# Optimization experiments

Measured on AMD Instinct MI355X. Metric: run time of the kernel, lower is better.

Reference implementation:

```python
import math
import jax, jax.numpy as jnp
import numpy as np

D_MODEL = 256
D2 = 2 * D_MODEL
NHEADS = 8
NLAYERS = 6
FFN = 1024
Q, B, S = 300, 16, 1024


def _ln(x, eps=1e-5):
    m = jnp.mean(x, axis=-1, keepdims=True)
    v = jnp.mean((x - m) ** 2, axis=-1, keepdims=True)
    return (x - m) / jnp.sqrt(v + eps)


def _mlp2(x, W1, b1, W2, b2):
    return jnp.maximum(x @ W1 + b1, 0.0) @ W2 + b2


def _sine_embed(pos, d_model):
    # pos: [Q, B, 2] -> [Q, B, d_model]
    fd = d_model // 2
    dim_t = jnp.arange(fd, dtype=jnp.float32)
    dim_t = 10000.0 ** (2.0 * jnp.floor(dim_t / 2.0) / fd)
    scale = 2.0 * math.pi
    px = (pos[:, :, 0] * scale)[:, :, None] / dim_t
    py = (pos[:, :, 1] * scale)[:, :, None] / dim_t

    def inter(p):
        q, b, _ = p.shape
        return jnp.stack((jnp.sin(p[:, :, 0::2]), jnp.cos(p[:, :, 1::2])), axis=3).reshape(q, b, -1)

    return jnp.concatenate((inter(py), inter(px)), axis=2)


def _pairwise_iou(b):
    # b: [B, Q, 4] xyxy -> [B, Q, Q]
    area = (b[..., 2] - b[..., 0]) * (b[..., 3] - b[..., 1])
    lt = jnp.maximum(b[:, :, None, :2], b[:, None, :, :2])
    rb = jnp.minimum(b[:, :, None, 2:], b[:, None, :, 2:])
    wh = jnp.clip(rb - lt, 0.0)
    inter = wh[..., 0] * wh[..., 1]
    union = area[:, :, None] + area[:, None, :] - inter
    return inter / union


def _mha(q, k, v, Wq, Wk, Wv, Wo, bias=None):
    # q: [L,B,D], k/v: [S,B,D]
    L, Bb, D = q.shape
    Ss = k.shape[0]
    hd = D // NHEADS
    qh = (q @ Wq).reshape(L, Bb, NHEADS, hd).transpose(1, 2, 0, 3)  # [B,H,L,hd]
    kh = (k @ Wk).reshape(Ss, Bb, NHEADS, hd).transpose(1, 2, 0, 3)
    vh = (v @ Wv).reshape(Ss, Bb, NHEADS, hd).transpose(1, 2, 0, 3)
    logits = jnp.einsum('bhqd,bhkd->bhqk', qh, kh) / jnp.sqrt(jnp.float32(hd))
    if bias is not None:
        logits = logits + bias[:, None]  # broadcast over heads
    a = jax.nn.softmax(logits, axis=-1)
    o = jnp.einsum('bhqk,bhkd->bhqd', a, vh).transpose(2, 0, 1, 3).reshape(L, Bb, D)
    return o @ Wo


def setup_inputs() -> dict:
    key = jax.random.key(0)
    ks = iter(jax.random.split(key, 40))
    f32 = jnp.float32
    d = D_MODEL
    sc = 0.02
    inp = {
        'tgt': jax.random.normal(next(ks), (Q, B, D2), f32),
        'memory': jax.random.normal(next(ks), (S, B, D2), f32),
        'pos': jax.random.normal(next(ks), (S, B, D2), f32),
        'query_pos': jax.random.normal(next(ks), (Q, B, d), f32),
        # query_scale MLP (d->d->d)
        'qs_W1': jax.random.normal(next(ks), (d, d), f32) * sc, 'qs_b1': jnp.zeros((d,), f32),
        'qs_W2': jax.random.normal(next(ks), (d, d), f32) * sc, 'qs_b2': jnp.zeros((d,), f32),
        # ref_point_head MLP (d->d->2)
        'rp_W1': jax.random.normal(next(ks), (d, d), f32) * sc, 'rp_b1': jnp.zeros((d,), f32),
        'rp_W2': jax.random.normal(next(ks), (d, 2), f32) * sc, 'rp_b2': jnp.zeros((2,), f32),
        # bbox_embed_func MLP (d->d->4)
        'bb_W1': jax.random.normal(next(ks), (d, d), f32) * sc, 'bb_b1': jnp.zeros((d,), f32),
        'bb_W2': jax.random.normal(next(ks), (d, 4), f32) * sc, 'bb_b2': jnp.zeros((4,), f32),
    }
    for name in ['sa_Wq', 'sa_Wk', 'sa_Wv', 'sa_Wo', 'ca_Wq', 'ca_Wk', 'ca_Wv', 'ca_Wo']:
        inp[name] = jax.random.normal(next(ks), (NLAYERS, D2, D2), f32) * sc
    inp['ff_W1'] = jax.random.normal(next(ks), (NLAYERS, D2, FFN), f32) * sc
    inp['ff_b1'] = jnp.zeros((NLAYERS, FFN), f32)
    inp['ff_W2'] = jax.random.normal(next(ks), (NLAYERS, FFN, D2), f32) * sc
    inp['ff_b2'] = jnp.zeros((NLAYERS, D2), f32)
    return inp


def reference(tgt, memory, pos, query_pos,
              qs_W1, qs_b1, qs_W2, qs_b2,
              rp_W1, rp_b1, rp_W2, rp_b2,
              bb_W1, bb_b1, bb_W2, bb_b2,
              sa_Wq, sa_Wk, sa_Wv, sa_Wo,
              ca_Wq, ca_Wk, ca_Wv, ca_Wo,
              ff_W1, ff_b1, ff_W2, ff_b2):
    d = D_MODEL
    output = tgt
    ref_before = _mlp2(query_pos, rp_W1, rp_b1, rp_W2, rp_b2)          # [Q,B,2]
    reference_points = jax.nn.sigmoid(ref_before).transpose(1, 0, 2)   # [B,Q,2]
    qp2 = jnp.concatenate((query_pos, query_pos), axis=-1)             # [Q,B,2d]
    for l in range(NLAYERS):
        obj_center = reference_points.transpose(1, 0, 2)               # [Q,B,2]
        pos_transform = _mlp2(output[..., d:], qs_W1, qs_b1, qs_W2, qs_b2)
        qs = _sine_embed(obj_center, d) * pos_transform                # [Q,B,d]
        tmp = _mlp2(output[..., d:], bb_W1, bb_b1, bb_W2, bb_b2)       # [Q,B,4]
        tmp = tmp.at[..., :2].add(ref_before)
        coord = jax.nn.sigmoid(tmp)                                    # cxcywh
        cx, cy, w, h = coord[..., 0], coord[..., 1], coord[..., 2], coord[..., 3]
        boxes = jnp.stack((cx - 0.5 * w, cy - 0.5 * h, cx + 0.5 * w, cy + 0.5 * h),
                          axis=-1).transpose(1, 0, 2)                  # [B,Q,4]
        gious = jax.lax.stop_gradient(_pairwise_iou(boxes))            # [B,Q,Q]
        cs = (cx + cy).transpose(1, 0)                                 # [B,Q]
        cxcys = jax.lax.stop_gradient((cs[:, :, None] > cs[:, None, :]).astype(output.dtype))
        bias = gious + cxcys                                            # [B,Q,Q]
        qs2 = jnp.concatenate((qs, qs), axis=-1)                        # [Q,B,2d]
        # self-attention with giou/cxcy bias
        qsa = output + qp2
        sa = _mha(qsa, qsa, output, sa_Wq[l], sa_Wk[l], sa_Wv[l], sa_Wo[l], bias=bias)
        output = _ln(output + sa)
        # cross-attention, sine-modulated query
        ca = _mha(output + qp2 + qs2, memory + pos, memory,
                  ca_Wq[l], ca_Wk[l], ca_Wv[l], ca_Wo[l])
        output = _ln(output + ca)
        ff = jnp.maximum(output @ ff_W1[l] + ff_b1[l], 0.0) @ ff_W2[l] + ff_b2[l]
        output = _ln(output + ff)
    return output[None]  # [1,Q,B,2d]
```

## Files before the change

### kernel.cpp

```cpp
#include <hip/hip_runtime.h>
#include <cmath>

#define QLEN 300
#define BATCH 16
#define SLEN 1024
#define DM 256
#define DD 512
#define FFND 1024
#define NQROWS (QLEN*BATCH)
#define NMROWS (SLEN*BATCH)
#define LQPAD 304
#define SAKPAD 320

typedef __attribute__((ext_vector_type(8))) short short8;
typedef __attribute__((ext_vector_type(4))) float f32x4;
typedef __attribute__((ext_vector_type(4))) unsigned short ushort4_;

__device__ __forceinline__ float sigmoidf_(float x){ return 1.f/(1.f+expf(-x)); }

__device__ __forceinline__ unsigned short f2bf(float x){
  unsigned u = __float_as_uint(x);
  unsigned r = (u + 0x7FFFu + ((u >> 16) & 1u)) >> 16;
  return (unsigned short)r;
}
__device__ __forceinline__ float bf2f(unsigned short u){
  return __uint_as_float(((unsigned)u) << 16);
}

__device__ __forceinline__ void gload16(const void* g, void* l) {
  __builtin_amdgcn_global_load_lds((const __attribute__((address_space(1))) unsigned int*)g,
                                   (__attribute__((address_space(3))) unsigned int*)l, 16, 0, 0);
}

__global__ __launch_bounds__(256) void transpose_cvt(
    const float* __restrict__ W, unsigned short* __restrict__ Wt, int K, int N)
{
  __shared__ float T[32][33];
  int n0 = blockIdx.x*32, k0 = blockIdx.y*32;
  size_t zo = (size_t)blockIdx.z * K * N;
  int tx = threadIdx.x & 31, ty = threadIdx.x >> 5;
  #pragma unroll
  for (int j = 0; j < 32; j += 8)
    T[ty+j][tx] = W[zo + (size_t)(k0+ty+j)*N + n0+tx];
  __syncthreads();
  #pragma unroll
  for (int j = 0; j < 32; j += 8)
    Wt[zo + (size_t)(n0+ty+j)*K + k0+tx] = f2bf(T[tx][ty+j]);
}

template<int BM, int OUTMODE, bool RELU>
__global__ __launch_bounds__(256) void gemm2(
    const unsigned short* __restrict__ Ab, const unsigned short* __restrict__ Wt,
    const float* __restrict__ bias, void* __restrict__ Cptr,
    int M, int N, int K, int lda, int Laux)
{
  __shared__ __align__(16) unsigned short As[2][BM*64];
  __shared__ __align__(16) unsigned short Bs[2][128*64];
  const int tid = threadIdx.x;
  const int w = tid >> 6, lane = tid & 63;
  const int bm = blockIdx.y*BM, bn = blockIdx.x*128;
  const int wm = w >> 1, wn = w & 1;
  const int c = lane & 15, hi = lane >> 4;
  constexpr int MR = BM/32;
  f32x4 acc[MR][4] = {};
  const int lrow8 = lane >> 3;
  const int lcol  = ((lane & 7) ^ lrow8) << 3;
  const int nt = K >> 6;

  auto stage = [&](int buf, int k0) {
    #pragma unroll
    for (int it = 0; it < BM/32; ++it) {
      int r = it*32 + w*8;
      gload16(&Ab[(size_t)(bm + r + lrow8)*lda + k0 + lcol], &As[buf][r*64]);
    }
    #pragma unroll
    for (int it = 0; it < 4; ++it) {
      int r = it*32 + w*8;
      gload16(&Wt[(size_t)(bn + r + lrow8)*K + k0 + lcol], &Bs[buf][r*64]);
    }
  };

  stage(0, 0);
  for (int t = 0; t < nt; ++t) {
    const int cur = t & 1;
    if (t + 1 < nt) {
      stage(cur ^ 1, (t+1) << 6);
      if constexpr (BM == 64) asm volatile("s_waitcnt vmcnt(6)" ::: "memory");
      else                    asm volatile("s_waitcnt vmcnt(8)" ::: "memory");
    } else {
      asm volatile("s_waitcnt vmcnt(0)" ::: "memory");
    }
    __builtin_amdgcn_s_barrier();
    #pragma unroll
    for (int ks = 0; ks < 2; ++ks) {
      short8 a[MR], bf[4];
      #pragma unroll
      for (int mr = 0; mr < MR; ++mr) {
        int m = wm*(BM/2) + mr*16 + c;
        a[mr] = *reinterpret_cast<const short8*>(&As[cur][m*64 + ((ks*32 + hi*8) ^ ((m&7)<<3))]);
      }
      #pragma unroll
      for (int nr = 0; nr < 4; ++nr) {
        int n = wn*64 + nr*16 + c;
        bf[nr] = *reinterpret_cast<const short8*>(&Bs[cur][n*64 + ((ks*32 + hi*8) ^ ((n&7)<<3))]);
      }
      #pragma unroll
      for (int mr = 0; mr < MR; ++mr)
        #pragma unroll
        for (int nr = 0; nr < 4; ++nr)
          acc[mr][nr] = __builtin_amdgcn_mfma_f32_16x16x32_bf16(a[mr], bf[nr], acc[mr][nr], 0, 0, 0);
    }
    asm volatile("s_waitcnt lgkmcnt(0)" ::: "memory");
    __builtin_amdgcn_sched_barrier(0);
    __builtin_amdgcn_s_barrier();
  }
  #pragma unroll
  for (int mr = 0; mr < MR; ++mr) {
    #pragma unroll
    for (int nr = 0; nr < 4; ++nr) {
      int colg = bn + wn*64 + nr*16 + c;
      float bv = bias ? bias[colg] : 0.f;
      #pragma unroll
      for (int r = 0; r < 4; ++r) {
        int rowg = bm + wm*(BM/2) + mr*16 + hi*4 + r;
        float v = acc[mr][nr][r] + bv;
        if (RELU) v = fmaxf(v, 0.f);
        if (OUTMODE == 0) {
          ((float*)Cptr)[(size_t)rowg*N + colg] = v;
        } else if (OUTMODE == 1) {
          ((unsigned short*)Cptr)[(size_t)rowg*N + colg] = f2bf(v);
        } else {
          int bb = rowg & 15, row = rowg >> 4, h = colg >> 6, dl = colg & 63;
          ((unsigned short*)Cptr)[(((size_t)bb*8 + h)*Laux + row)*64 + dl] = f2bf(v);
        }
      }
    }
  }
}

template<int BM>
__global__ __launch_bounds__(256) void gemm2_vt(
    const unsigned short* __restrict__ Ab, const unsigned short* __restrict__ Wt,
    unsigned short* __restrict__ VT, int Lsrc, int K, int lda, int Lkpad, int tilesPerB)
{
  __shared__ __align__(16) unsigned short As[2][BM*64];
  __shared__ __align__(16) unsigned short Bs[2][128*64];
  const int tid = threadIdx.x;
  const int w = tid >> 6, lane = tid & 63;
  const int b = blockIdx.y / tilesPerB;
  const int qt = (blockIdx.y - b*tilesPerB) * BM;
  const int bn = blockIdx.x*128;
  const int wm = w >> 1, wn = w & 1;
  const int c = lane & 15, hi = lane >> 4;
  constexpr int MR = BM/32;
  f32x4 acc[MR][4] = {};
  const int lrow8 = lane >> 3;
  const int lcol  = ((lane & 7) ^ lrow8) << 3;
  const int nt = K >> 6;

  auto stage = [&](int buf, int k0) {
    #pragma unroll
    for (int it = 0; it < BM/32; ++it) {
      int r = it*32 + w*8;
      int q = qt + r + lrow8; if (q > Lsrc-1) q = Lsrc-1;
      gload16(&Ab[(size_t)(q*BATCH + b)*lda + k0 + lcol], &As[buf][r*64]);
    }
    #pragma unroll
    for (int it = 0; it < 4; ++it) {
      int r = it*32 + w*8;
      gload16(&Wt[(size_t)(bn + r + lrow8)*K + k0 + lcol], &Bs[buf][r*64]);
    }
  };

  stage(0, 0);
  for (int t = 0; t < nt; ++t) {
    const int cur = t & 1;
    if (t + 1 < nt) {
      stage(cur ^ 1, (t+1) << 6);
      if constexpr (BM == 64) asm volatile("s_waitcnt vmcnt(6)" ::: "memory");
      else                    asm volatile("s_waitcnt vmcnt(8)" ::: "memory");
    } else {
      asm volatile("s_waitcnt vmcnt(0)" ::: "memory");
    }
    __builtin_amdgcn_s_barrier();
    #pragma unroll
    for (int ks = 0; ks < 2; ++ks) {
      short8 a[MR], bf[4];
      #pragma unroll
      for (int mr = 0; mr < MR; ++mr) {
        int m = wm*(BM/2) + mr*16 + c;
        a[mr] = *reinterpret_cast<const short8*>(&As[cur][m*64 + ((ks*32 + hi*8) ^ ((m&7)<<3))]);
      }
      #pragma unroll
      for (int nr = 0; nr < 4; ++nr) {
        int n = wn*64 + nr*16 + c;
        bf[nr] = *reinterpret_cast<const short8*>(&Bs[cur][n*64 + ((ks*32 + hi*8) ^ ((n&7)<<3))]);
      }
      #pragma unroll
      for (int mr = 0; mr < MR; ++mr)
        #pragma unroll
        for (int nr = 0; nr < 4; ++nr)
          acc[mr][nr] = __builtin_amdgcn_mfma_f32_16x16x32_bf16(a[mr], bf[nr], acc[mr][nr], 0, 0, 0);
    }
    asm volatile("s_waitcnt lgkmcnt(0)" ::: "memory");
    __builtin_amdgcn_sched_barrier(0);
    __builtin_amdgcn_s_barrier();
  }
  #pragma unroll
  for (int mr = 0; mr < MR; ++mr) {
    #pragma unroll
    for (int nr = 0; nr < 4; ++nr) {
      int colg = bn + wn*64 + nr*16 + c;
      int h = colg >> 6, dl = colg & 63;
      int q0 = qt + wm*(BM/2) + mr*16 + hi*4;
      ushort4_ pack;
      #pragma unroll
      for (int r = 0; r < 4; ++r) pack[r] = f2bf(acc[mr][nr][r]);
      *reinterpret_cast<ushort4_*>(&VT[((size_t)(b*8 + h)*64 + dl)*Lkpad + q0]) = pack;
    }
  }
}

template<int AMODE, bool OUTBF16, bool RELU>
__global__ __launch_bounds__(256) void gemm_mfma(
    const void* __restrict__ Aptr, const float* __restrict__ A2,
    const unsigned short* __restrict__ Wt, const float* __restrict__ bias,
    void* __restrict__ Cptr, int M, int N, int K, int lda)
{
  __shared__ __align__(16) unsigned short As[64][72];
  __shared__ __align__(16) unsigned short Bs[64][72];
  const int tid = threadIdx.x;
  const int bm = blockIdx.y*64, bn = blockIdx.x*64;
  const int w = tid >> 6, lane = tid & 63;
  const int wm = w >> 1, wn = w & 1;
  const int c = lane & 15, hi = lane >> 4;
  const int sr = tid >> 3, sk = (tid & 7) * 8;
  f32x4 acc[2][2] = {};
  for (int k0 = 0; k0 < K; k0 += 64) {
    #pragma unroll
    for (int it = 0; it < 2; ++it) {
      int m = sr + it*32;
      if (AMODE == 0) {
        const unsigned short* Ab = (const unsigned short*)Aptr;
        short8 v = *reinterpret_cast<const short8*>(&Ab[(size_t)(bm+m)*lda + k0 + sk]);
        *reinterpret_cast<short8*>(&As[m][sk]) = v;
      } else {
        const float* Af = (const float*)Aptr;
        size_t base = (size_t)(bm+m)*lda + k0 + sk;
        float4 f0 = *reinterpret_cast<const float4*>(&Af[base]);
        float4 f1 = *reinterpret_cast<const float4*>(&Af[base+4]);
        short8 v;
        v[0]=(short)f2bf(f0.x); v[1]=(short)f2bf(f0.y); v[2]=(short)f2bf(f0.z); v[3]=(short)f2bf(f0.w);
        v[4]=(short)f2bf(f1.x); v[5]=(short)f2bf(f1.y); v[6]=(short)f2bf(f1.z); v[7]=(short)f2bf(f1.w);
        *reinterpret_cast<short8*>(&As[m][sk]) = v;
      }
      short8 bv = *reinterpret_cast<const short8*>(&Wt[(size_t)(bn+m)*K + k0 + sk]);
      *reinterpret_cast<short8*>(&Bs[m][sk]) = bv;
    }
    __syncthreads();
    #pragma unroll
    for (int ks = 0; ks < 2; ++ks) {
      short8 a0 = *reinterpret_cast<const short8*>(&As[wm*32 + c][ks*32 + hi*8]);
      short8 a1 = *reinterpret_cast<const short8*>(&As[wm*32 + 16 + c][ks*32 + hi*8]);
      short8 b0 = *reinterpret_cast<const short8*>(&Bs[wn*32 + c][ks*32 + hi*8]);
      short8 b1 = *reinterpret_cast<const short8*>(&Bs[wn*32 + 16 + c][ks*32 + hi*8]);
      acc[0][0] = __builtin_amdgcn_mfma_f32_16x16x32_bf16(a0, b0, acc[0][0], 0, 0, 0);
      acc[0][1] = __builtin_amdgcn_mfma_f32_16x16x32_bf16(a0, b1, acc[0][1], 0, 0, 0);
      acc[1][0] = __builtin_amdgcn_mfma_f32_16x16x32_bf16(a1, b0, acc[1][0], 0, 0, 0);
      acc[1][1] = __builtin_amdgcn_mfma_f32_16x16x32_bf16(a1, b1, acc[1][1], 0, 0, 0);
    }
    __syncthreads();
  }
  #pragma unroll
  for (int mf = 0; mf < 2; ++mf) {
    #pragma unroll
    for (int nf = 0; nf < 2; ++nf) {
      int colg = bn + wn*32 + nf*16 + c;
      float bv = bias ? bias[colg] : 0.f;
      #pragma unroll
      for (int r = 0; r < 4; ++r) {
        int rowg = bm + wm*32 + mf*16 + hi*4 + r;
        float v = acc[mf][nf][r] + bv;
        if (RELU) v = fmaxf(v, 0.f);
        if (OUTBF16) ((unsigned short*)Cptr)[(size_t)rowg*N + colg] = f2bf(v);
        else         ((float*)Cptr)[(size_t)rowg*N + colg] = v;
      }
    }
  }
}

template<bool HAS_BIAS, bool MASK, int NS>
__global__ __launch_bounds__(256) void attn2(
    const unsigned short* __restrict__ Qh, const unsigned short* __restrict__ Kh,
    const unsigned short* __restrict__ VT, const float* __restrict__ bias,
    unsigned short* __restrict__ Ob, unsigned short* __restrict__ Opart, float* __restrict__ MLpart,
    int Lq, int Lk, int Lkpad)
{
  __shared__ __align__(16) unsigned short Ks[2][64*64];
  __shared__ __align__(16) unsigned short Vs[2][64*64];
  __shared__ __align__(16) unsigned short Pl[4][16][72];
  const int tid = threadIdx.x;
  const int w = tid >> 6, lane = tid & 63;
  const int c = lane & 15, hi = lane >> 4;
  const int bh = blockIdx.x;
  const int qt = blockIdx.y * 64;
  const int sp = blockIdx.z;
  const int b = bh >> 3;
  const int lrow8 = lane >> 3;
  const int lcol  = ((lane & 7) ^ lrow8) << 3;

  const int nt_tot = (Lk + 63) >> 6;
  const int t0 = (nt_tot * sp) / NS;
  const int t1 = (nt_tot * (sp + 1)) / NS;

  int qrow = qt + w*16 + c; if (qrow > Lq-1) qrow = Lq-1;
  const unsigned short* qptr = Qh + ((size_t)bh*Lq + qrow)*64;
  short8 qf0 = *reinterpret_cast<const short8*>(qptr + hi*8);
  short8 qf1 = *reinterpret_cast<const short8*>(qptr + 32 + hi*8);

  float m_ = -1e30f, l_ = 0.f;
  f32x4 accO[4] = {};
  const int qbase = qt + w*16 + hi*4;

  auto stageKV = [&](int buf, int kt) {
    #pragma unroll
    for (int it = 0; it < 2; ++it) {
      int r = it*32 + w*8;
      int kr = kt + r + lrow8; if (MASK && kr > Lk-1) kr = Lk-1;
      gload16(&Kh[((size_t)bh*Lk + kr)*64 + lcol], &Ks[buf][r*64]);
    }
    #pragma unroll
    for (int it = 0; it < 2; ++it) {
      int r = it*32 + w*8;
      gload16(&VT[((size_t)bh*64 + r + lrow8)*Lkpad + kt + lcol], &Vs[buf][r*64]);
    }
  };

  stageKV(0, t0 << 6);
  for (int t = t0; t < t1; ++t) {
    const int cur = (t - t0) & 1;
    const int kt = t << 6;
    float4 bs4[4];
    if (HAS_BIAS) {
      #pragma unroll
      for (int g = 0; g < 4; ++g)
        bs4[g] = *reinterpret_cast<const float4*>(
            &bias[((size_t)b*Lq + qrow)*Lk + kt + g*16 + hi*4]);
    }
    if (t + 1 < t1) {
      stageKV(cur ^ 1, (t+1) << 6);
      asm volatile("s_waitcnt vmcnt(4)" ::: "memory");
    } else {
      asm volatile("s_waitcnt vmcnt(0)" ::: "memory");
    }
    __builtin_amdgcn_s_barrier();
    f32x4 s[4] = {};
    #pragma unroll
    for (int g = 0; g < 4; ++g) {
      int m = g*16 + c;
      short8 kb0 = *reinterpret_cast<const short8*>(&Ks[cur][m*64 + ((hi*8)      ^ ((m&7)<<3))]);
      short8 kb1 = *reinterpret_cast<const short8*>(&Ks[cur][m*64 + ((32 + hi*8) ^ ((m&7)<<3))]);
      s[g] = __builtin_amdgcn_mfma_f32_16x16x32_bf16(kb0, qf0, s[g], 0, 0, 0);
      s[g] = __builtin_amdgcn_mfma_f32_16x16x32_bf16(kb1, qf1, s[g], 0, 0, 0);
    }
    float tmax = -1e30f;
    #pragma unroll
    for (int g = 0; g < 4; ++g) {
      #pragma unroll
      for (int r = 0; r < 4; ++r) {
        float v = s[g][r] * 0.125f;
        if (HAS_BIAS) v += ((const float*)&bs4[g])[r];
        if (MASK && (kt + g*16 + hi*4 + r >= Lk)) v = -1e30f;
        s[g][r] = v;
        tmax = fmaxf(tmax, v);
      }
    }
    tmax = fmaxf(tmax, __shfl_xor(tmax, 16));
    tmax = fmaxf(tmax, __shfl_xor(tmax, 32));
    float newm = fmaxf(m_, tmax);
    float corr = __expf(m_ - newm);
    m_ = newm;
    float psum = 0.f;
    #pragma unroll
    for (int g = 0; g < 4; ++g) {
      ushort4_ pp;
      #pragma unroll
      for (int r = 0; r < 4; ++r) {
        float e = __expf(s[g][r] - newm);
        psum += e;
        pp[r] = f2bf(e);
      }
      *reinterpret_cast<ushort4_*>(&Pl[w][c][g*16 + hi*4]) = pp;
    }
    psum += __shfl_xor(psum, 16);
    psum += __shfl_xor(psum, 32);
    l_ = l_*corr + psum;
    float corr4[4];
    #pragma unroll
    for (int r = 0; r < 4; ++r) corr4[r] = __shfl(corr, hi*4 + r);
    #pragma unroll
    for (int dg = 0; dg < 4; ++dg)
      #pragma unroll
      for (int r = 0; r < 4; ++r) accO[dg][r] *= corr4[r];
    #pragma unroll
    for (int ks = 0; ks < 2; ++ks) {
      short8 pa = *reinterpret_cast<const short8*>(&Pl[w][c][ks*32 + hi*8]);
      #pragma unroll
      for (int dg = 0; dg < 4; ++dg) {
        int n = dg*16 + c;
        short8 vb = *reinterpret_cast<const short8*>(&Vs[cur][n*64 + ((ks*32 + hi*8) ^ ((n&7)<<3))]);
        accO[dg] = __builtin_amdgcn_mfma_f32_16x16x32_bf16(pa, vb, accO[dg], 0, 0, 0);
      }
    }
    asm volatile("s_waitcnt lgkmcnt(0)" ::: "memory");
    __builtin_amdgcn_sched_barrier(0);
    __builtin_amdgcn_s_barrier();
  }
  if (NS == 1) {
    float l4[4];
    #pragma unroll
    for (int r = 0; r < 4; ++r) l4[r] = __shfl(l_, hi*4 + r);
    #pragma unroll
    for (int r = 0; r < 4; ++r) {
      int qg = qbase + r;
      if (qg < Lq) {
        float inv = 1.f / l4[r];
        int h = bh & 7;
        #pragma unroll
        for (int dg = 0; dg < 4; ++dg)
          Ob[((size_t)qg*BATCH + b)*DD + h*64 + 16*dg + c] = f2bf(accO[dg][r] * inv);
      }
    }
  } else {
    int qc = qt + w*16 + c;
    if (hi == 0 && qc < Lq) {
      size_t rowml = ((size_t)sp*128 + bh)*LQPAD + qc;
      MLpart[rowml*2]     = m_;
      MLpart[rowml*2 + 1] = l_;
    }
    #pragma unroll
    for (int r = 0; r < 4; ++r) {
      int qg = qbase + r;
      if (qg < Lq) {
        size_t rowo = ((size_t)sp*128 + bh)*LQPAD + qg;
        #pragma unroll
        for (int dg = 0; dg < 4; ++dg)
          Opart[rowo*64 + dg*16 + c] = f2bf(accO[dg][r]);
      }
    }
  }
}

__global__ __launch_bounds__(256) void attn_reduce(
    const unsigned short* __restrict__ Opart, const float* __restrict__ MLpart,
    unsigned short* __restrict__ Ob, int Lq)
{
  int w = threadIdx.x >> 6, lane = threadIdx.x & 63;
  int pair = blockIdx.x*4 + w;
  if (pair >= 128*Lq) return;
  int bh = pair / Lq, q = pair - bh*Lq;
  size_t r0 = (size_t)bh*LQPAD + q;
  size_t r1 = (size_t)(128 + bh)*LQPAD + q;
  float m0 = MLpart[r0*2], l0 = MLpart[r0*2+1];
  float m1 = MLpart[r1*2], l1 = MLpart[r1*2+1];
  float M = fmaxf(m0, m1);
  float w0 = __expf(m0 - M), w1 = __expf(m1 - M);
  float o = w0*bf2f(Opart[r0*64 + lane]) + w1*bf2f(Opart[r1*64 + lane]);
  float l = w0*l0 + w1*l1;
  int b = bh >> 3, h = bh & 7;
  Ob[((size_t)q*BATCH + b)*DD + h*64 + lane] = f2bf(o / l);
}

__global__ __launch_bounds__(256) void gemm_f32(
    const float* __restrict__ A, const float* __restrict__ A2,
    const float* __restrict__ W, const float* __restrict__ bias,
    float* __restrict__ C, int M, int N, int K, int lda, int relu)
{
  __shared__ __align__(16) float As[16][68];
  __shared__ __align__(16) float Bs[16][68];
  const int tid = threadIdx.x;
  const int bm = blockIdx.y * 64, bn = blockIdx.x * 64;
  const int tx = tid & 15, ty = tid >> 4;
  const int ar = tid >> 4, ac = tid & 15;
  const int bk = tid >> 6, bnn = tid & 63;
  float acc[4][4] = {};
  for (int k0 = 0; k0 < K; k0 += 16) {
    #pragma unroll
    for (int i = 0; i < 4; ++i) {
      int row = ar + i*16;
      float v = A[(size_t)(bm+row)*lda + (k0+ac)];
      if (A2) v += A2[(size_t)(bm+row)*lda + (k0+ac)];
      As[ac][row] = v;
    }
    #pragma unroll
    for (int i = 0; i < 4; ++i) {
      int kk = bk + i*4;
      Bs[kk][bnn] = W[(size_t)(k0+kk)*N + (bn+bnn)];
    }
    __syncthreads();
    #pragma unroll
    for (int k = 0; k < 16; ++k) {
      float4 a4 = *reinterpret_cast<const float4*>(&As[k][ty*4]);
      float4 b4 = *reinterpret_cast<const float4*>(&Bs[k][tx*4]);
      float a[4] = {a4.x,a4.y,a4.z,a4.w};
      float bb[4] = {b4.x,b4.y,b4.z,b4.w};
      #pragma unroll
      for (int i=0;i<4;++i)
        #pragma unroll
        for (int j=0;j<4;++j)
          acc[i][j] = fmaf(a[i], bb[j], acc[i][j]);
// ... 115 lines not shown
  float4 p0 = *reinterpret_cast<const float4*>(pos+base);
  float4 p1 = *reinterpret_cast<const float4*>(pos+base+4);
  short8 s1, s2;
  s1[0]=(short)f2bf(a0.x+p0.x); s1[1]=(short)f2bf(a0.y+p0.y); s1[2]=(short)f2bf(a0.z+p0.z); s1[3]=(short)f2bf(a0.w+p0.w);
  s1[4]=(short)f2bf(a1.x+p1.x); s1[5]=(short)f2bf(a1.y+p1.y); s1[6]=(short)f2bf(a1.z+p1.z); s1[7]=(short)f2bf(a1.w+p1.w);
  s2[0]=(short)f2bf(a0.x); s2[1]=(short)f2bf(a0.y); s2[2]=(short)f2bf(a0.z); s2[3]=(short)f2bf(a0.w);
  s2[4]=(short)f2bf(a1.x); s2[5]=(short)f2bf(a1.y); s2[6]=(short)f2bf(a1.z); s2[7]=(short)f2bf(a1.w);
  *reinterpret_cast<short8*>(mb+base)  = s1;
  *reinterpret_cast<short8*>(mvb+base) = s2;
}

__global__ __launch_bounds__(256) void ln_residual(float* __restrict__ X, const float* __restrict__ Y,
                                                   unsigned short* __restrict__ Xb)
{
  int row = blockIdx.x, tid = threadIdx.x;
  size_t base = (size_t)row*DD;
  float v0 = X[base+tid]     + Y[base+tid];
  float v1 = X[base+tid+256] + Y[base+tid+256];
  float s = v0+v1, sq = v0*v0+v1*v1;
  for (int off = 32; off; off >>= 1) { s += __shfl_down(s,off); sq += __shfl_down(sq,off); }
  __shared__ float ss[4], ssq[4];
  int wid = tid>>6, lane = tid&63;
  if (lane==0){ ss[wid]=s; ssq[wid]=sq; }
  __syncthreads();
  if (tid==0){
    float a=ss[0]+ss[1]+ss[2]+ss[3], bsum=ssq[0]+ssq[1]+ssq[2]+ssq[3];
    float mean = a*(1.f/DD);
    float var  = bsum*(1.f/DD) - mean*mean;
    ss[0]=mean; ssq[0]=rsqrtf(fmaxf(var,0.f)+1e-5f);
  }
  __syncthreads();
  float mean = ss[0], inv = ssq[0];
  float o0 = (v0-mean)*inv, o1 = (v1-mean)*inv;
  X[base+tid]     = o0;  Xb[base+tid]     = f2bf(o0);
  X[base+tid+256] = o1;  Xb[base+tid+256] = f2bf(o1);
}

__global__ void init_x(const float* __restrict__ t, float* __restrict__ X,
                       unsigned short* __restrict__ Xb, int n)
{
  int idx = blockIdx.x*blockDim.x + threadIdx.x;
  if (idx < n){ float v = t[idx]; X[idx]=v; Xb[idx]=f2bf(v); }
}

__global__ void copy_f32(const float* __restrict__ src, float* __restrict__ dst, int n)
{
  int idx = blockIdx.x*blockDim.x + threadIdx.x;
  if (idx < n) dst[idx] = src[idx];
}

extern "C" void kernel_launch(void* const* d_in, const int* in_sizes, int n_in,
                              void* d_out, int out_size, void* d_ws, size_t ws_size,
                              hipStream_t stream)
{
  const float* tgt       = (const float*)d_in[0];
  const float* memory    = (const float*)d_in[1];
  const float* pos       = (const float*)d_in[2];
  const float* query_pos = (const float*)d_in[3];
  const float* qs_W1 = (const float*)d_in[4];  const float* qs_b1 = (const float*)d_in[5];
  const float* qs_W2 = (const float*)d_in[6];  const float* qs_b2 = (const float*)d_in[7];
  const float* rp_W1 = (const float*)d_in[8];  const float* rp_b1 = (const float*)d_in[9];
  const float* rp_W2 = (const float*)d_in[10]; const float* rp_b2 = (const float*)d_in[11];
  const float* bb_W1 = (const float*)d_in[12]; const float* bb_b1 = (const float*)d_in[13];
  const float* bb_W2 = (const float*)d_in[14]; const float* bb_b2 = (const float*)d_in[15];
  const float* sa_Wq = (const float*)d_in[16]; const float* sa_Wk = (const float*)d_in[17];
  const float* sa_Wv = (const float*)d_in[18]; const float* sa_Wo = (const float*)d_in[19];
  const float* ca_Wq = (const float*)d_in[20]; const float* ca_Wk = (const float*)d_in[21];
  const float* ca_Wv = (const float*)d_in[22]; const float* ca_Wo = (const float*)d_in[23];
  const float* ff_W1 = (const float*)d_in[24]; const float* ff_b1 = (const float*)d_in[25];
  const float* ff_W2 = (const float*)d_in[26]; const float* ff_b2 = (const float*)d_in[27];

  float* F = (float*)d_ws;
  size_t o = 0;
  float* X    = F + o; o += (size_t)NQROWS*DD;
  float* RES  = F + o; o += (size_t)NQROWS*DD;
  float* SINE = F + o; o += (size_t)NQROWS*DM;
  float* PT   = F + o; o += (size_t)NQROWS*DM;
  float* BIAS = F + o; o += (size_t)BATCH*QLEN*QLEN;
  float* REFB = F + o; o += (size_t)NQROWS*2;
  float* T4   = F + o; o += (size_t)NQROWS*4;
  float* BOX  = F + o; o += (size_t)NQROWS*4;
  float* CS   = F + o; o += (size_t)NQROWS;
  float* ML   = F + o; o += (size_t)2*128*LQPAD*2;
  float* T256 = RES;
  unsigned short* U = (unsigned short*)(F + o);
  size_t u = 0;
  unsigned short* Xb   = U + u; u += (size_t)NQROWS*DD;
  unsigned short* QIN  = U + u; u += (size_t)NQROWS*DD;
  unsigned short* PQb  = U + u; u += (size_t)NQROWS*DD;
  unsigned short* PKb  = U + u; u += (size_t)NMROWS*DD;
  unsigned short* PVb  = U + u; u += (size_t)NMROWS*DD;
  unsigned short* VTsa = U + u; u += (size_t)128*64*SAKPAD;
  unsigned short* OPARTU = U + u; u += (size_t)2*128*LQPAD*64;
  unsigned short* T256b= U + u; u += (size_t)NQROWS*DM;
  unsigned short* MEMb = U + u; u += (size_t)NMROWS*DD;
  unsigned short* MEMVb= U + u; u += (size_t)NMROWS*DD;
  unsigned short* WtSq = U + u; u += (size_t)6*DD*DD;
  unsigned short* WtSk = U + u; u += (size_t)6*DD*DD;
  unsigned short* WtSv = U + u; u += (size_t)6*DD*DD;
  unsigned short* WtSo = U + u; u += (size_t)6*DD*DD;
  unsigned short* WtCq = U + u; u += (size_t)6*DD*DD;
  unsigned short* WtCk = U + u; u += (size_t)6*DD*DD;
  unsigned short* WtCv = U + u; u += (size_t)6*DD*DD;
  unsigned short* WtCo = U + u; u += (size_t)6*DD*DD;
  unsigned short* WtF1 = U + u; u += (size_t)6*DD*FFND;
  unsigned short* WtF2 = U + u; u += (size_t)6*DD*FFND;
  unsigned short* WtQ1 = U + u; u += (size_t)DM*DM;
  unsigned short* WtQ2 = U + u; u += (size_t)DM*DM;
  unsigned short* WtB1 = U + u; u += (size_t)DM*DM;
  unsigned short* AOb  = QIN;
  unsigned short* HIDb = PKb;
  if (ws_size < o*sizeof(float) + u*sizeof(unsigned short)) return;

  dim3 B256(256);
  const int nTotal = NQROWS*DD;

  transpose_cvt<<<dim3(16,16,6), B256, 0, stream>>>(sa_Wq, WtSq, DD, DD);
  transpose_cvt<<<dim3(16,16,6), B256, 0, stream>>>(sa_Wk, WtSk, DD, DD);
  transpose_cvt<<<dim3(16,16,6), B256, 0, stream>>>(sa_Wv, WtSv, DD, DD);
  transpose_cvt<<<dim3(16,16,6), B256, 0, stream>>>(sa_Wo, WtSo, DD, DD);
  transpose_cvt<<<dim3(16,16,6), B256, 0, stream>>>(ca_Wq, WtCq, DD, DD);
  transpose_cvt<<<dim3(16,16,6), B256, 0, stream>>>(ca_Wk, WtCk, DD, DD);
  transpose_cvt<<<dim3(16,16,6), B256, 0, stream>>>(ca_Wv, WtCv, DD, DD);
  transpose_cvt<<<dim3(16,16,6), B256, 0, stream>>>(ca_Wo, WtCo, DD, DD);
  transpose_cvt<<<dim3(32,16,6), B256, 0, stream>>>(ff_W1, WtF1, DD, FFND);
  transpose_cvt<<<dim3(16,32,6), B256, 0, stream>>>(ff_W2, WtF2, FFND, DD);
  transpose_cvt<<<dim3(8,8,1),  B256, 0, stream>>>(qs_W1, WtQ1, DM, DM);
  transpose_cvt<<<dim3(8,8,1),  B256, 0, stream>>>(qs_W2, WtQ2, DM, DM);
  transpose_cvt<<<dim3(8,8,1),  B256, 0, stream>>>(bb_W1, WtB1, DM, DM);

  init_x<<<dim3((nTotal+255)/256), B256, 0, stream>>>(tgt, X, Xb, nTotal);
  cvt_mem<<<dim3(NMROWS*DD/8/256), B256, 0, stream>>>(memory, pos, MEMb, MEMVb);
  gemm_f32<<<dim3(DM/64, NQROWS/64), B256, 0, stream>>>(query_pos, nullptr, rp_W1, rp_b1, T256, NQROWS, DM, DM, DM, 1);
  gemm_skinny<<<dim3(NQROWS/4), B256, 0, stream>>>(T256, rp_W2, rp_b2, REFB, NQROWS, 2, DM, DM);
  sine_embed_kernel<<<dim3((NQROWS*DM+255)/256), B256, 0, stream>>>(REFB, SINE);

  const int nredu = (128*QLEN + 3) / 4;
  const int qtiles = (QLEN + 63) / 64;
  for (int l = 0; l < 6; ++l) {
    const size_t wo = (size_t)l*DD*DD, fo = (size_t)l*DD*FFND;
    const float* fb1 = ff_b1 + (size_t)l*FFND;
    const float* fb2 = ff_b2 + (size_t)l*DD;

    gemm_mfma<0,true,true ><<<dim3(DM/64, NQROWS/64), B256, 0, stream>>>(Xb+DM, nullptr, WtQ1, qs_b1, T256b, NQROWS, DM, DM, DD);
    gemm_mfma<0,false,false><<<dim3(DM/64, NQROWS/64), B256, 0, stream>>>(T256b, nullptr, WtQ2, qs_b2, PT, NQROWS, DM, DM, DM);
    gemm_mfma<0,false,true ><<<dim3(DM/64, NQROWS/64), B256, 0, stream>>>(Xb+DM, nullptr, WtB1, bb_b1, T256, NQROWS, DM, DM, DD);
    gemm_skinny<<<dim3(NQROWS/4), B256, 0, stream>>>(T256, bb_W2, bb_b2, T4, NQROWS, 4, DM, DM);
    boxes_kernel<<<dim3((NQROWS+255)/256), B256, 0, stream>>>(T4, REFB, BOX, CS);
    bias_kernel<<<dim3((BATCH*QLEN*QLEN+255)/256), B256, 0, stream>>>(BOX, CS, BIAS);

    add_qp2<<<dim3((nTotal+255)/256), B256, 0, stream>>>(X, query_pos, QIN);
    gemm2<64,2,false><<<dim3(DD/128, NQROWS/64), B256, 0, stream>>>(QIN, WtSq+wo, nullptr, PQb, NQROWS, DD, DD, DD, QLEN);
    gemm2<64,2,false><<<dim3(DD/128, NQROWS/64), B256, 0, stream>>>(QIN, WtSk+wo, nullptr, PKb, NQROWS, DD, DD, DD, QLEN);
    gemm2_vt<64><<<dim3(DD/128, BATCH*5), B256, 0, stream>>>(Xb, WtSv+wo, VTsa, QLEN, DD, DD, SAKPAD, 5);
    attn2<true,true,2><<<dim3(128, qtiles, 2), B256, 0, stream>>>(PQb, PKb, VTsa, BIAS, nullptr, OPARTU, ML, QLEN, QLEN, SAKPAD);
    attn_reduce<<<dim3(nredu), B256, 0, stream>>>(OPARTU, ML, AOb, QLEN);
    gemm2<64,0,false><<<dim3(DD/128, NQROWS/64), B256, 0, stream>>>(AOb, WtSo+wo, nullptr, RES, NQROWS, DD, DD, DD, 0);
    ln_residual<<<dim3(NQROWS), B256, 0, stream>>>(X, RES, Xb);

    caq_kernel<<<dim3((nTotal+255)/256), B256, 0, stream>>>(X, query_pos, SINE, PT, QIN);
    gemm2<64,2,false><<<dim3(DD/128, NQROWS/64), B256, 0, stream>>>(QIN, WtCq+wo, nullptr, PQb, NQROWS, DD, DD, DD, QLEN);
    gemm2<128,2,false><<<dim3(DD/128, NMROWS/128), B256, 0, stream>>>(MEMb,  WtCk+wo, nullptr, PKb, NMROWS, DD, DD, DD, SLEN);
    gemm2_vt<128><<<dim3(DD/128, BATCH*8), B256, 0, stream>>>(MEMVb, WtCv+wo, PVb, SLEN, DD, DD, SLEN, 8);
    attn2<false,false,2><<<dim3(128, qtiles, 2), B256, 0, stream>>>(PQb, PKb, PVb, nullptr, nullptr, OPARTU, ML, QLEN, SLEN, SLEN);
    attn_reduce<<<dim3(nredu), B256, 0, stream>>>(OPARTU, ML, AOb, QLEN);
    gemm2<64,0,false><<<dim3(DD/128, NQROWS/64), B256, 0, stream>>>(AOb, WtCo+wo, nullptr, RES, NQROWS, DD, DD, DD, 0);
    ln_residual<<<dim3(NQROWS), B256, 0, stream>>>(X, RES, Xb);

    gemm2<64,1,true ><<<dim3(FFND/128, NQROWS/64), B256, 0, stream>>>(Xb, WtF1+fo, fb1, HIDb, NQROWS, FFND, DD, DD, 0);
    gemm2<64,0,false><<<dim3(DD/128, NQROWS/64), B256, 0, stream>>>(HIDb, WtF2+fo, fb2, RES, NQROWS, DD, FFND, FFND, 0);
    ln_residual<<<dim3(NQROWS), B256, 0, stream>>>(X, RES, Xb);
  }

  copy_f32<<<dim3((nTotal+255)/256), B256, 0, stream>>>(X, (float*)d_out, out_size);
}
```

Measured before the change: 1.767 ms.

## Fuse Q/K projections and query MLP first layers, shrink GEMM tiles, add MFMA priority

Self-attention Q and K projection weights are packed into one interleaved matrix so a single GEMM writes both head-major outputs, and attention takes per-batch stride and offset parameters to read them. The qs/bb first-layer MLPs are merged into one split-output GEMM with a concatenated bias. Several N=512 GEMMs switch to a 32-row tile to launch more blocks, and attention raises wave priority around its MFMA sections. This removes kernel launches and re-reads of the input in exchange for new indexing paths; the BM=32 path's staging and waitcnt correctness is unverified.

```diff
diff --git a/kernel.cpp b/kernel.cpp
--- a/kernel.cpp
+++ b/kernel.cpp
@@ -33,19 +33,29 @@
 }
 
 __global__ __launch_bounds__(256) void transpose_cvt(
-    const float* __restrict__ W, unsigned short* __restrict__ Wt, int K, int N)
+    const float* __restrict__ W, unsigned short* __restrict__ Wt, int K, int N,
+    size_t zsrc, size_t zdst)
 {
   __shared__ float T[32][33];
   int n0 = blockIdx.x*32, k0 = blockIdx.y*32;
-  size_t zo = (size_t)blockIdx.z * K * N;
+  size_t zs = (size_t)blockIdx.z * zsrc;
+  size_t zd = (size_t)blockIdx.z * zdst;
   int tx = threadIdx.x & 31, ty = threadIdx.x >> 5;
   #pragma unroll
   for (int j = 0; j < 32; j += 8)
-    T[ty+j][tx] = W[zo + (size_t)(k0+ty+j)*N + n0+tx];
+    T[ty+j][tx] = W[zs + (size_t)(k0+ty+j)*N + n0+tx];
   __syncthreads();
   #pragma unroll
   for (int j = 0; j < 32; j += 8)
-    Wt[zo + (size_t)(n0+ty+j)*K + k0+tx] = f2bf(T[tx][ty+j]);
+    Wt[zd + (size_t)(n0+ty+j)*K + k0+tx] = f2bf(T[tx][ty+j]);
+}
+
+__global__ void concat_bias(const float* __restrict__ b1, const float* __restrict__ b2,
+                            float* __restrict__ out)
+{
+  int i = blockIdx.x*256 + threadIdx.x;
+  if (i < 256) out[i] = b1[i];
+  else if (i < 512) out[i] = b2[i-256];
 }
 
 template<int BM, int OUTMODE, bool RELU>
@@ -61,8 +71,8 @@
   const int bm = blockIdx.y*BM, bn = blockIdx.x*128;
   const int wm = w >> 1, wn = w & 1;
   const int c = lane & 15, hi = lane >> 4;
-  constexpr int MR = BM/32;
-  f32x4 acc[MR][4] = {};
+  constexpr int MR = (BM + 31)/32 < 1 ? 1 : BM/32;
+  f32x4 acc[MR < 1 ? 1 : MR][4] = {};
   const int lrow8 = lane >> 3;
   const int lcol  = ((lane & 7) ^ lrow8) << 3;
   const int nt = K >> 6;
@@ -85,8 +95,9 @@
     const int cur = t & 1;
     if (t + 1 < nt) {
       stage(cur ^ 1, (t+1) << 6);
-      if constexpr (BM == 64) asm volatile("s_waitcnt vmcnt(6)" ::: "memory");
-      else                    asm volatile("s_waitcnt vmcnt(8)" ::: "memory");
+      if constexpr (BM == 32)      asm volatile("s_waitcnt vmcnt(5)" ::: "memory");
+      else if constexpr (BM == 64) asm volatile("s_waitcnt vmcnt(6)" ::: "memory");
+      else                         asm volatile("s_waitcnt vmcnt(8)" ::: "memory");
     } else {
       asm volatile("s_waitcnt vmcnt(0)" ::: "memory");
     }
@@ -114,6 +125,7 @@
     __builtin_amdgcn_sched_barrier(0);
     __builtin_amdgcn_s_barrier();
   }
+  const int hs = N >> 6;
   #pragma unroll
   for (int mr = 0; mr < MR; ++mr) {
     #pragma unroll
@@ -131,7 +143,7 @@
           ((unsigned short*)Cptr)[(size_t)rowg*N + colg] = f2bf(v);
         } else {
           int bb = rowg & 15, row = rowg >> 4, h = colg >> 6, dl = colg & 63;
-          ((unsigned short*)Cptr)[(((size_t)bb*8 + h)*Laux + row)*64 + dl] = f2bf(v);
+          ((unsigned short*)Cptr)[(((size_t)bb*hs + h)*Laux + row)*64 + dl] = f2bf(v);
         }
       }
     }
@@ -289,12 +301,66 @@
   }
 }
 
+__global__ __launch_bounds__(256) void gemm_mfma_split(
+    const unsigned short* __restrict__ Ab, const unsigned short* __restrict__ Wt,
+    const float* __restrict__ bias, unsigned short* __restrict__ C1, float* __restrict__ C2,
+    int M, int N, int K, int lda)
+{
+  __shared__ __align__(16) unsigned short As[64][72];
+  __shared__ __align__(16) unsigned short Bs[64][72];
+  const int tid = threadIdx.x;
+  const int bm = blockIdx.y*64, bn = blockIdx.x*64;
+  const int w = tid >> 6, lane = tid & 63;
+  const int wm = w >> 1, wn = w & 1;
+  const int c = lane & 15, hi = lane >> 4;
+  const int sr = tid >> 3, sk = (tid & 7) * 8;
+  f32x4 acc[2][2] = {};
+  for (int k0 = 0; k0 < K; k0 += 64) {
+    #pragma unroll
+    for (int it = 0; it < 2; ++it) {
+      int m = sr + it*32;
+      short8 v = *reinterpret_cast<const short8*>(&Ab[(size_t)(bm+m)*lda + k0 + sk]);
+      *reinterpret_cast<short8*>(&As[m][sk]) = v;
+      short8 bv = *reinterpret_cast<const short8*>(&Wt[(size_t)(bn+m)*K + k0 + sk]);
+      *reinterpret_cast<short8*>(&Bs[m][sk]) = bv;
+    }
+    __syncthreads();
+    #pragma unroll
+    for (int ks = 0; ks < 2; ++ks) {
+      short8 a0 = *reinterpret_cast<const short8*>(&As[wm*32 + c][ks*32 + hi*8]);
+      short8 a1 = *reinterpret_cast<const short8*>(&As[wm*32 + 16 + c][ks*32 + hi*8]);
+      short8 b0 = *reinterpret_cast<const short8*>(&Bs[wn*32 + c][ks*32 + hi*8]);
+      short8 b1 = *reinterpret_cast<const short8*>(&Bs[wn*32 + 16 + c][ks*32 + hi*8]);
+      acc[0][0] = __builtin_amdgcn_mfma_f32_16x16x32_bf16(a0, b0, acc[0][0], 0, 0, 0);
+      acc[0][1] = __builtin_amdgcn_mfma_f32_16x16x32_bf16(a0, b1, acc[0][1], 0, 0, 0);
+      acc[1][0] = __builtin_amdgcn_mfma_f32_16x16x32_bf16(a1, b0, acc[1][0], 0, 0, 0);
+      acc[1][1] = __builtin_amdgcn_mfma_f32_16x16x32_bf16(a1, b1, acc[1][1], 0, 0, 0);
+    }
+    __syncthreads();
+  }
+  #pragma unroll
+  for (int mf = 0; mf < 2; ++mf) {
+    #pragma unroll
+    for (int nf = 0; nf < 2; ++nf) {
+      int colg = bn + wn*32 + nf*16 + c;
+      float bv = bias[colg];
+      #pragma unroll
+      for (int r = 0; r < 4; ++r) {
+        int rowg = bm + wm*32 + mf*16 + hi*4 + r;
+        float v = fmaxf(acc[mf][nf][r] + bv, 0.f);
+        if (colg < 256) C1[(size_t)rowg*256 + colg] = f2bf(v);
+        else            C2[(size_t)rowg*256 + (colg-256)] = v;
+      }
+    }
+  }
+}
+
 template<bool HAS_BIAS, bool MASK, int NS>
 __global__ __launch_bounds__(256) void attn2(
     const unsigned short* __restrict__ Qh, const unsigned short* __restrict__ Kh,
     const unsigned short* __restrict__ VT, const float* __restrict__ bias,
     unsigned short* __restrict__ Ob, unsigned short* __restrict__ Opart, float* __restrict__ MLpart,
-    int Lq, int Lk, int Lkpad)
+    int Lq, int Lk, int Lkpad, int qmul, int kmul, int koff)
 {
   __shared__ __align__(16) unsigned short Ks[2][64*64];
   __shared__ __align__(16) unsigned short Vs[2][64*64];
@@ -305,7 +371,7 @@
   const int bh = blockIdx.x;
   const int qt = blockIdx.y * 64;
   const int sp = blockIdx.z;
-  const int b = bh >> 3;
+  const int b = bh >> 3, h = bh & 7;
   const int lrow8 = lane >> 3;
   const int lcol  = ((lane & 7) ^ lrow8) << 3;
 
@@ -314,9 +380,10 @@
   const int t1 = (nt_tot * (sp + 1)) / NS;
 
   int qrow = qt + w*16 + c; if (qrow > Lq-1) qrow = Lq-1;
-  const unsigned short* qptr = Qh + ((size_t)bh*Lq + qrow)*64;
+  const unsigned short* qptr = Qh + ((size_t)(b*qmul + h)*Lq + qrow)*64;
   short8 qf0 = *reinterpret_cast<const short8*>(qptr + hi*8);
   short8 qf1 = *reinterpret_cast<const short8*>(qptr + 32 + hi*8);
+  const size_t kbase = (size_t)(b*kmul + koff + h)*Lk;
 
   float m_ = -1e30f, l_ = 0.f;
   f32x4 accO[4] = {};
@@ -327,7 +394,7 @@
     for (int it = 0; it < 2; ++it) {
       int r = it*32 + w*8;
       int kr = kt + r + lrow8; if (MASK && kr > Lk-1) kr = Lk-1;
-      gload16(&Kh[((size_t)bh*Lk + kr)*64 + lcol], &Ks[buf][r*64]);
+      gload16(&Kh[(kbase + kr)*64 + lcol], &Ks[buf][r*64]);
     }
     #pragma unroll
     for (int it = 0; it < 2; ++it) {
@@ -355,6 +422,7 @@
     }
     __builtin_amdgcn_s_barrier();
     f32x4 s[4] = {};
+    __builtin_amdgcn_s_setprio(1);
     #pragma unroll
     for (int g = 0; g < 4; ++g) {
       int m = g*16 + c;
@@ -363,6 +431,7 @@
       s[g] = __builtin_amdgcn_mfma_f32_16x16x32_bf16(kb0, qf0, s[g], 0, 0, 0);
       s[g] = __builtin_amdgcn_mfma_f32_16x16x32_bf16(kb1, qf1, s[g], 0, 0, 0);
     }
+    __builtin_amdgcn_s_setprio(0);
     float tmax = -1e30f;
     #pragma unroll
     for (int g = 0; g < 4; ++g) {
@@ -402,6 +471,7 @@
     for (int dg = 0; dg < 4; ++dg)
       #pragma unroll
       for (int r = 0; r < 4; ++r) accO[dg][r] *= corr4[r];
+    __builtin_amdgcn_s_setprio(1);
     #pragma unroll
     for (int ks = 0; ks < 2; ++ks) {
       short8 pa = *reinterpret_cast<const short8*>(&Pl[w][c][ks*32 + hi*8]);
@@ -412,6 +482,7 @@
         accO[dg] = __builtin_amdgcn_mfma_f32_16x16x32_bf16(pa, vb, accO[dg], 0, 0, 0);
       }
     }
+    __builtin_amdgcn_s_setprio(0);
     asm volatile("s_waitcnt lgkmcnt(0)" ::: "memory");
     __builtin_amdgcn_sched_barrier(0);
     __builtin_amdgcn_s_barrier();
@@ -425,7 +496,6 @@
       int qg = qbase + r;
       if (qg < Lq) {
         float inv = 1.f / l4[r];
-        int h = bh & 7;
         #pragma unroll
         for (int dg = 0; dg < 4; ++dg)
           Ob[((size_t)qg*BATCH + b)*DD + h*64 + 16*dg + c] = f2bf(accO[dg][r] * inv);
@@ -707,6 +777,7 @@
   float* BOX  = F + o; o += (size_t)NQROWS*4;
   float* CS   = F + o; o += (size_t)NQROWS;
   float* ML   = F + o; o += (size_t)2*128*LQPAD*2;
+  float* QBB  = F + o; o += 512;
   float* T256 = RES;
   unsigned short* U = (unsigned short*)(F + o);
   size_t u = 0;
@@ -720,8 +791,7 @@
   unsigned short* T256b= U + u; u += (size_t)NQROWS*DM;
   unsigned short* MEMb = U + u; u += (size_t)NMROWS*DD;
   unsigned short* MEMVb= U + u; u += (size_t)NMROWS*DD;
-  unsigned short* WtSq = U + u; u += (size_t)6*DD*DD;
-  unsigned short* WtSk = U + u; u += (size_t)6*DD*DD;
+  unsigned short* WtSqk= U + u; u += (size_t)6*2*DD*DD;
   unsigned short* WtSv = U + u; u += (size_t)6*DD*DD;
   unsigned short* WtSo = U + u; u += (size_t)6*DD*DD;
   unsigned short* WtCq = U + u; u += (size_t)6*DD*DD;
@@ -730,29 +800,31 @@
   unsigned short* WtCo = U + u; u += (size_t)6*DD*DD;
   unsigned short* WtF1 = U + u; u += (size_t)6*DD*FFND;
   unsigned short* WtF2 = U + u; u += (size_t)6*DD*FFND;
-  unsigned short* WtQ1 = U + u; u += (size_t)DM*DM;
+  unsigned short* WtQB = U + u; u += (size_t)2*DM*DM;
   unsigned short* WtQ2 = U + u; u += (size_t)DM*DM;
-  unsigned short* WtB1 = U + u; u += (size_t)DM*DM;
+  unsigned short* QKb  = PQb;
   unsigned short* AOb  = QIN;
   unsigned short* HIDb = PKb;
   if (ws_size < o*sizeof(float) + u*sizeof(unsigned short)) return;
 
   dim3 B256(256);
   const int nTotal = NQROWS*DD;
-
-  transpose_cvt<<<dim3(16,16,6), B256, 0, stream>>>(sa_Wq, WtSq, DD, DD);
-  transpose_cvt<<<dim3(16,16,6), B256, 0, stream>>>(sa_Wk, WtSk, DD, DD);
-  transpose_cvt<<<dim3(16,16,6), B256, 0, stream>>>(sa_Wv, WtSv, DD, DD);
-  transpose_cvt<<<dim3(16,16,6), B256, 0, stream>>>(sa_Wo, WtSo, DD, DD);
-  transpose_cvt<<<dim3(16,16,6), B256, 0, stream>>>(ca_Wq, WtCq, DD, DD);
-  transpose_cvt<<<dim3(16,16,6), B256, 0, stream>>>(ca_Wk, WtCk, DD, DD);
-  transpose_cvt<<<dim3(16,16,6), B256, 0, stream>>>(ca_Wv, WtCv, DD, DD);
-  transpose_cvt<<<dim3(16,16,6), B256, 0, stream>>>(ca_Wo, WtCo, DD, DD);
-  transpose_cvt<<<dim3(32,16,6), B256, 0, stream>>>(ff_W1, WtF1, DD, FFND);
-  transpose_cvt<<<dim3(16,32,6), B256, 0, stream>>>(ff_W2, WtF2, FFND, DD);
-  transpose_cvt<<<dim3(8,8,1),  B256, 0, stream>>>(qs_W1, WtQ1, DM, DM);
-  transpose_cvt<<<dim3(8,8,1),  B256, 0, stream>>>(qs_W2, WtQ2, DM, DM);
-  transpose_cvt<<<dim3(8,8,1),  B256, 0, stream>>>(bb_W1, WtB1, DM, DM);
+  const size_t ZD = (size_t)DD*DD;
+
+  transpose_cvt<<<dim3(16,16,6), B256, 0, stream>>>(sa_Wq, WtSqk,      DD, DD, ZD, 2*ZD);
+  transpose_cvt<<<dim3(16,16,6), B256, 0, stream>>>(sa_Wk, WtSqk + ZD, DD, DD, ZD, 2*ZD);
+  transpose_cvt<<<dim3(16,16,6), B256, 0, stream>>>(sa_Wv, WtSv, DD, DD, ZD, ZD);
+  transpose_cvt<<<dim3(16,16,6), B256, 0, stream>>>(sa_Wo, WtSo, DD, DD, ZD, ZD);
+  transpose_cvt<<<dim3(16,16,6), B256, 0, stream>>>(ca_Wq, WtCq, DD, DD, ZD, ZD);
+  transpose_cvt<<<dim3(16,16,6), B256, 0, stream>>>(ca_Wk, WtCk, DD, DD, ZD, ZD);
+  transpose_cvt<<<dim3(16,16,6), B256, 0, stream>>>(ca_Wv, WtCv, DD, DD, ZD, ZD);
+  transpose_cvt<<<dim3(16,16,6), B256, 0, stream>>>(ca_Wo, WtCo, DD, DD, ZD, ZD);
+  transpose_cvt<<<dim3(32,16,6), B256, 0, stream>>>(ff_W1, WtF1, DD, FFND, (size_t)DD*FFND, (size_t)DD*FFND);
+  transpose_cvt<<<dim3(16,32,6), B256, 0, stream>>>(ff_W2, WtF2, FFND, DD, (size_t)DD*FFND, (size_t)DD*FFND);
+  transpose_cvt<<<dim3(8,8,1),  B256, 0, stream>>>(qs_W1, WtQB,             DM, DM, (size_t)DM*DM, (size_t)DM*DM);
+  transpose_cvt<<<dim3(8,8,1),  B256, 0, stream>>>(bb_W1, WtQB + (size_t)DM*DM, DM, DM, (size_t)DM*DM, (size_t)DM*DM);
+  transpose_cvt<<<dim3(8,8,1),  B256, 0, stream>>>(qs_W2, WtQ2, DM, DM, (size_t)DM*DM, (size_t)DM*DM);
+  concat_bias<<<dim3(2), B256, 0, stream>>>(qs_b1, bb_b1, QBB);
 
   init_x<<<dim3((nTotal+255)/256), B256, 0, stream>>>(tgt, X, Xb, nTotal);
   cvt_mem<<<dim3(NMROWS*DD/8/256), B256, 0, stream>>>(memory, pos, MEMb, MEMVb);
@@ -767,33 +839,31 @@
     const float* fb1 = ff_b1 + (size_t)l*FFND;
     const float* fb2 = ff_b2 + (size_t)l*DD;
 
-    gemm_mfma<0,true,true ><<<dim3(DM/64, NQROWS/64), B256, 0, stream>>>(Xb+DM, nullptr, WtQ1, qs_b1, T256b, NQROWS, DM, DM, DD);
+    gemm_mfma_split<<<dim3(8, NQROWS/64), B256, 0, stream>>>(Xb+DM, WtQB, QBB, T256b, T256, NQROWS, 512, DM, DD);
     gemm_mfma<0,false,false><<<dim3(DM/64, NQROWS/64), B256, 0, stream>>>(T256b, nullptr, WtQ2, qs_b2, PT, NQROWS, DM, DM, DM);
-    gemm_mfma<0,false,true ><<<dim3(DM/64, NQROWS/64), B256, 0, stream>>>(Xb+DM, nullptr, WtB1, bb_b1, T256, NQROWS, DM, DM, DD);
     gemm_skinny<<<dim3(NQROWS/4), B256, 0, stream>>>(T256, bb_W2, bb_b2, T4, NQROWS, 4, DM, DM);
     boxes_kernel<<<dim3((NQROWS+255)/256), B256, 0, stream>>>(T4, REFB, BOX, CS);
     bias_kernel<<<dim3((BATCH*QLEN*QLEN+255)/256), B256, 0, stream>>>(BOX, CS, BIAS);
 
     add_qp2<<<dim3((nTotal+255)/256), B256, 0, stream>>>(X, query_pos, QIN);
-    gemm2<64,2,false><<<dim3(DD/128, NQROWS/64), B256, 0, stream>>>(QIN, WtSq+wo, nullptr, PQb, NQROWS, DD, DD, DD, QLEN);
-    gemm2<64,2,false><<<dim3(DD/128, NQROWS/64), B256, 0, stream>>>(QIN, WtSk+wo, nullptr, PKb, NQROWS, DD, DD, DD, QLEN);
+    gemm2<64,2,false><<<dim3(1024/128, NQROWS/64), B256, 0, stream>>>(QIN, WtSqk + (size_t)l*2*ZD, nullptr, QKb, NQROWS, 1024, DD, DD, QLEN);
     gemm2_vt<64><<<dim3(DD/128, BATCH*5), B256, 0, stream>>>(Xb, WtSv+wo, VTsa, QLEN, DD, DD, SAKPAD, 5);
-    attn2<true,true,2><<<dim3(128, qtiles, 2), B256, 0, stream>>>(PQb, PKb, VTsa, BIAS, nullptr, OPARTU, ML, QLEN, QLEN, SAKPAD);
+    attn2<true,true,2><<<dim3(128, qtiles, 2), B256, 0, stream>>>(QKb, QKb, VTsa, BIAS, nullptr, OPARTU, ML, QLEN, QLEN, SAKPAD, 16, 16, 8);
     attn_reduce<<<dim3(nredu), B256, 0, stream>>>(OPARTU, ML, AOb, QLEN);
-    gemm2<64,0,false><<<dim3(DD/128, NQROWS/64), B256, 0, stream>>>(AOb, WtSo+wo, nullptr, RES, NQROWS, DD, DD, DD, 0);
+    gemm2<32,0,false><<<dim3(DD/128, NQROWS/32), B256, 0, stream>>>(AOb, WtSo+wo, nullptr, RES, NQROWS, DD, DD, DD, 0);
     ln_residual<<<dim3(NQROWS), B256, 0, stream>>>(X, RES, Xb);
 
     caq_kernel<<<dim3((nTotal+255)/256), B256, 0, stream>>>(X, query_pos, SINE, PT, QIN);
-    gemm2<64,2,false><<<dim3(DD/128, NQROWS/64), B256, 0, stream>>>(QIN, WtCq+wo, nullptr, PQb, NQROWS, DD, DD, DD, QLEN);
+    gemm2<32,2,false><<<dim3(DD/128, NQROWS/32), B256, 0, stream>>>(QIN, WtCq+wo, nullptr, PQb, NQROWS, DD, DD, DD, QLEN);
     gemm2<128,2,false><<<dim3(DD/128, NMROWS/128), B256, 0, stream>>>(MEMb,  WtCk+wo, nullptr, PKb, NMROWS, DD, DD, DD, SLEN);
     gemm2_vt<128><<<dim3(DD/128, BATCH*8), B256, 0, stream>>>(MEMVb, WtCv+wo, PVb, SLEN, DD, DD, SLEN, 8);
-    attn2<false,false,2><<<dim3(128, qtiles, 2), B256, 0, stream>>>(PQb, PKb, PVb, nullptr, nullptr, OPARTU, ML, QLEN, SLEN, SLEN);
+    attn2<false,false,2><<<dim3(128, qtiles, 2), B256, 0, stream>>>(PQb, PKb, PVb, nullptr, nullptr, OPARTU, ML, QLEN, SLEN, SLEN, 8, 8, 0);
     attn_reduce<<<dim3(nredu), B256, 0, stream>>>(OPARTU, ML, AOb, QLEN);
-    gemm2<64,0,false><<<dim3(DD/128, NQROWS/64), B256, 0, stream>>>(AOb, WtCo+wo, nullptr, RES, NQROWS, DD, DD, DD, 0);
+    gemm2<32,0,false><<<dim3(DD/128, NQROWS/32), B256, 0, stream>>>(AOb, WtCo+wo, nullptr, RES, NQROWS, DD, DD, DD, 0);
     ln_residual<<<dim3(NQROWS), B256, 0, stream>>>(X, RES, Xb);
 
     gemm2<64,1,true ><<<dim3(FFND/128, NQROWS/64), B256, 0, stream>>>(Xb, WtF1+fo, fb1, HIDb, NQROWS, FFND, DD, DD, 0);
-    gemm2<64,0,false><<<dim3(DD/128, NQROWS/64), B256, 0, stream>>>(HIDb, WtF2+fo, fb2, RES, NQROWS, DD, FFND, FFND, 0);
+    gemm2<32,0,false><<<dim3(DD/128, NQROWS/32), B256, 0, stream>>>(HIDb, WtF2+fo, fb2, RES, NQROWS, DD, FFND, FFND, 0);
     ln_residual<<<dim3(NQROWS), B256, 0, stream>>>(X, RES, Xb);
   }
 
```

Measured after the change: 1.657 ms. -6.2%, faster.
